# Performance work log

Measured on AMD Instinct MI355X. Metric: run time of the kernel, lower is better.

## Reference

```python
import jax, jax.numpy as jnp
import numpy as np

B, FIXED_LEN, N_FRAME, MID, P = 4096, 8192, 2112, 264, 88
UNROLLED_ITER = 5


def setup_inputs() -> dict:
    key = jax.random.key(0)
    ks = jax.random.split(key, 8)
    # Fourier weights scaled by 1/FIXED_LEN as in fourier_init
    W_cos = jax.random.normal(ks[0], (N_FRAME, FIXED_LEN), jnp.float32) / FIXED_LEN
    W_sin = jax.random.normal(ks[1], (N_FRAME, FIXED_LEN), jnp.float32) / FIXED_LEN
    # template is |cisoid_dict|^2 >= 0; small positive values keep the unrolled loop stable
    template = jax.random.uniform(ks[2], (N_FRAME, MID), jnp.float32) * 0.01
    return {
        "input_this": jax.random.normal(ks[3], (B, FIXED_LEN), jnp.float32),
        "input_prev": jax.random.normal(ks[4], (B, FIXED_LEN), jnp.float32),
        "W_cos": W_cos,
        "W_sin": W_sin,
        "template": template,
        "W1": jax.random.normal(ks[5], (MID, MID), jnp.float32) * 0.05 + jnp.eye(MID, dtype=jnp.float32),
        "b1": jnp.zeros((MID,), jnp.float32),
        "W2": jax.random.normal(ks[6], (P, MID), jnp.float32) * 0.1,
        "b2": jnp.zeros((P,), jnp.float32),
        "Wout": jax.random.normal(ks[7], (P, P), jnp.float32) * 0.1 + 4.0 * jnp.eye(P, dtype=jnp.float32),
        "bout": jnp.full((P,), -3.0, jnp.float32),
    }


def reference(input_this, input_prev, W_cos, W_sin, template, W1, b1, W2, b2, Wout, bout):
    fixed_len = jnp.asarray(input_this.shape[1], input_this.dtype)
    # get_feat: normalized power spectrum features
    n_valid = (jnp.count_nonzero(input_this, axis=1) + 1).astype(input_this.dtype)[:, None]
    scale = fixed_len / n_valid                      # [B, 1]
    x_cos = (input_this @ W_cos.T) * scale           # [B, N_FRAME]
    x_sin = (input_this @ W_sin.T) * scale
    feat = x_cos * x_cos + x_sin * x_sin             # [B, N_FRAME]

    # process_feat: unrolled LISTA-style iterations
    running = feat
    xi = -running
    m = jax.nn.relu(-10.0 * (xi @ template))         # [B, MID]
    for _ in range(UNROLLED_ITER - 1):
        xi = 1.6 * ((m @ template.T) - running) + 0.2 * xi
        m = jax.nn.relu(-8.0 * (xi @ template) + 0.2 * m)

    h = jax.nn.relu(jax.nn.relu(m @ W1.T + b1) @ W2.T + b2)  # [B, P]
    return jax.nn.sigmoid(h @ Wout.T + bout)         # velocity_estimate [B, P]
```

## Files before the change

kernel.cpp:

```cpp
#include <hip/hip_runtime.h>
#include <cstdint>
#include <cstddef>

#define B_SZ 4096
#define KLEN 8192
#define NF   2112
#define MID  264
#define PD   88

typedef _Float16 f16;
typedef _Float16 f16x4 __attribute__((ext_vector_type(4)));
typedef _Float16 f16x8 __attribute__((ext_vector_type(8)));
typedef float    f32x4 __attribute__((ext_vector_type(4)));

__device__ __forceinline__ void gl2lds16(const void* g, void* l) {
    __builtin_amdgcn_global_load_lds(
        (const __attribute__((address_space(1))) void*)g,
        (__attribute__((address_space(3))) void*)l, 16, 0, 0);
}

__global__ void k_row_prep(const float* __restrict__ x, f16* __restrict__ xh,
                           float* __restrict__ alpha) {
    const int row = blockIdx.x;
    const float* xr = x + (size_t)row * KLEN;
    f16* xhr = xh + (size_t)row * KLEN;
    int cnt = 0;
    for (int j = threadIdx.x * 4; j < KLEN; j += 256 * 4) {
        float4 v = *(const float4*)(xr + j);
        f16x4 h = { (f16)v.x, (f16)v.y, (f16)v.z, (f16)v.w };
        *(f16x4*)(xhr + j) = h;
        cnt += (v.x != 0.f) + (v.y != 0.f) + (v.z != 0.f) + (v.w != 0.f);
    }
    for (int off = 32; off > 0; off >>= 1) cnt += __shfl_down(cnt, off);
    __shared__ int lsum[4];
    if ((threadIdx.x & 63) == 0) lsum[threadIdx.x >> 6] = cnt;
    __syncthreads();
    if (threadIdx.x == 0)
        alpha[row] = 8.0f / (float)(lsum[0] + lsum[1] + lsum[2] + lsum[3] + 1);
}

__global__ void k_cvt_w2(const float* __restrict__ wc, const float* __restrict__ ws,
                         f16* __restrict__ whc, f16* __restrict__ whs, int n4) {
    const float* w = blockIdx.y ? ws : wc;
    f16* wh = blockIdx.y ? whs : whc;
    for (int i = blockIdx.x * blockDim.x + threadIdx.x; i < n4; i += gridDim.x * blockDim.x) {
        float4 v = ((const float4*)w)[i];
        f16x4 h = { (f16)(v.x * 8192.f), (f16)(v.y * 8192.f),
                    (f16)(v.z * 8192.f), (f16)(v.w * 8192.f) };
        ((f16x4*)wh)[i] = h;
    }
}

__global__ void k_prep_tt(const float* __restrict__ T, f16* __restrict__ tt) {
    __shared__ float tile[32][33];
    const int k0 = blockIdx.x * 32, n0 = blockIdx.y * 32;
    const int tx = threadIdx.x & 31, ty = threadIdx.x >> 5;
    for (int r = ty; r < 32; r += 8) {
        const int k = k0 + r, n = n0 + tx;
        tile[r][tx] = (n < MID) ? T[(size_t)k * MID + n] : 0.f;
    }
    __syncthreads();
    for (int r = ty; r < 32; r += 8) {
        const int n = n0 + r, k = k0 + tx;
        tt[(size_t)n * NF + k] = (f16)tile[tx][r];
    }
}

__global__ void k_gram(const float* __restrict__ T, float* __restrict__ G) {
    __shared__ float Pp[32][64];
    __shared__ float Qq[32][64];
    const int i0 = blockIdx.x * 64, j0 = blockIdx.y * 64;
    const int tx = threadIdx.x & 15, ty = threadIdx.x >> 4;
    float acc[4][4] = {};
    for (int kc = blockIdx.z * 11; kc < (int)blockIdx.z * 11 + 11; ++kc) {
        const int k0 = kc * 32;
        for (int l = threadIdx.x; l < 32 * 64; l += 256) {
            const int kk = l >> 6, cc = l & 63, kr = k0 + kk;
            Pp[kk][cc] = (i0 + cc < MID) ? T[(size_t)kr * MID + i0 + cc] : 0.f;
            Qq[kk][cc] = (j0 + cc < MID) ? T[(size_t)kr * MID + j0 + cc] : 0.f;
        }
        __syncthreads();
        for (int kk = 0; kk < 32; ++kk) {
            float a_[4], b_[4];
#pragma unroll
            for (int u = 0; u < 4; ++u) a_[u] = Pp[kk][tx * 4 + u];
#pragma unroll
            for (int w = 0; w < 4; ++w) b_[w] = Qq[kk][ty * 4 + w];
#pragma unroll
            for (int u = 0; u < 4; ++u)
#pragma unroll
                for (int w = 0; w < 4; ++w) acc[u][w] += a_[u] * b_[w];
        }
        __syncthreads();
    }
    for (int u = 0; u < 4; ++u) {
        const int gi = i0 + tx * 4 + u;
        if (gi >= MID) continue;
        for (int w = 0; w < 4; ++w) {
            const int gj = j0 + ty * 4 + w;
            if (gj < MID) atomicAdd(&G[(size_t)gi * MID + gj], acc[u][w]);
        }
    }
}

__global__ __launch_bounds__(256, 2) void k_fourier(
    const f16* __restrict__ A, const f16* __restrict__ Bc, const f16* __restrict__ Bs,
    const float* __restrict__ alpha, f16* __restrict__ feat) {
    __shared__ __align__(16) f16 As4[4][128 * 32];
    __shared__ __align__(16) f16 Bcs4[4][64 * 32];
    __shared__ __align__(16) f16 Bss4[4][64 * 32];
    const int tid = threadIdx.x, lane = tid & 63, wave = tid >> 6;
    const int wm = wave & 1, wn = wave >> 1;

    const int bid = blockIdx.y * 33 + blockIdx.x;
    const int swz = (bid & 7) * 132 + (bid >> 3);
    const int bx = swz % 33, by = swz / 33;
    const int m0 = by * 128, n0 = bx * 64;

    const int srow = tid >> 2;
    const int cswz = ((tid & 3) ^ ((tid >> 3) & 3)) << 3;
    const f16* pA  = A  + (size_t)(m0 + srow) * KLEN + cswz;
    const f16* pBc = Bc + (size_t)(n0 + srow) * KLEN + cswz;
    const f16* pBs = Bs + (size_t)(n0 + srow) * KLEN + cswz;

#define STAGE_F(h, b)                                                             \
    {                                                                             \
        gl2lds16(pA + (size_t)(h) * 32, (char*)&As4[b][0] + tid * 16);            \
        gl2lds16(pA + (size_t)64 * KLEN + (size_t)(h) * 32,                       \
                 (char*)&As4[b][0] + (tid + 256) * 16);                           \
        gl2lds16(pBc + (size_t)(h) * 32, (char*)&Bcs4[b][0] + tid * 16);          \
        gl2lds16(pBs + (size_t)(h) * 32, (char*)&Bss4[b][0] + tid * 16);          \
    }

    const int c0 = lane >> 4;
    int offA[4], offB[2];
#pragma unroll
    for (int mt = 0; mt < 4; ++mt) {
        const int r = wm * 64 + mt * 16 + (lane & 15);
        offA[mt] = r * 32 + ((c0 ^ ((r >> 1) & 3)) << 3);
    }
#pragma unroll
    for (int nt = 0; nt < 2; ++nt) {
        const int r = wn * 32 + nt * 16 + (lane & 15);
        offB[nt] = r * 32 + ((c0 ^ ((r >> 1) & 3)) << 3);
    }

    f32x4 accC[4][2], accS[4][2];
    const f32x4 z4 = {0.f, 0.f, 0.f, 0.f};
#pragma unroll
    for (int i = 0; i < 4; ++i)
#pragma unroll
        for (int j = 0; j < 2; ++j) { accC[i][j] = z4; accS[i][j] = z4; }

#define COMPUTE_F(b)                                                              \
    {                                                                             \
        f16x8 af[4], bcf[2], bsf[2];                                              \
        _Pragma("unroll")                                                         \
        for (int mt = 0; mt < 4; ++mt)                                            \
            af[mt] = *(const f16x8*)(&As4[b][offA[mt]]);                          \
        _Pragma("unroll")                                                         \
        for (int nt = 0; nt < 2; ++nt) {                                          \
            bcf[nt] = *(const f16x8*)(&Bcs4[b][offB[nt]]);                        \
            bsf[nt] = *(const f16x8*)(&Bss4[b][offB[nt]]);                        \
        }                                                                         \
        __builtin_amdgcn_s_setprio(1);                                            \
        _Pragma("unroll")                                                         \
        for (int mt = 0; mt < 4; ++mt)                                            \
            _Pragma("unroll")                                                     \
            for (int nt = 0; nt < 2; ++nt) {                                      \
                accC[mt][nt] = __builtin_amdgcn_mfma_f32_16x16x32_f16(            \
                    af[mt], bcf[nt], accC[mt][nt], 0, 0, 0);                      \
                accS[mt][nt] = __builtin_amdgcn_mfma_f32_16x16x32_f16(            \
                    af[mt], bsf[nt], accS[mt][nt], 0, 0, 0);                      \
            }                                                                     \
        __builtin_amdgcn_s_setprio(0);                                            \
    }

#define WAITB(n)                                                                  \
    asm volatile("s_waitcnt vmcnt(" #n ")" ::: "memory");                         \
    __builtin_amdgcn_s_barrier();

    STAGE_F(0, 0); STAGE_F(1, 1); STAGE_F(2, 2);
    WAITB(8);

#pragma unroll 1
    for (int h = 0; h < 252; h += 4) {
        STAGE_F(h + 3, 3); COMPUTE_F(0); WAITB(8);
        STAGE_F(h + 4, 0); COMPUTE_F(1); WAITB(8);
        STAGE_F(h + 5, 1); COMPUTE_F(2); WAITB(8);
        STAGE_F(h + 6, 2); COMPUTE_F(3); WAITB(8);
    }
    STAGE_F(255, 3); COMPUTE_F(0); WAITB(8);
    COMPUTE_F(1); WAITB(4);
    COMPUTE_F(2); WAITB(0);
    COMPUTE_F(3);
#undef STAGE_F
#undef COMPUTE_F
#undef WAITB

#pragma unroll
    for (int mt = 0; mt < 4; ++mt)
#pragma unroll
        for (int reg = 0; reg < 4; ++reg) {
            const int row = m0 + wm * 64 + mt * 16 + ((lane >> 4) << 2) + reg;
            const float al = alpha[row];
#pragma unroll
            for (int nt = 0; nt < 2; ++nt) {
                const int col = n0 + wn * 32 + nt * 16 + (lane & 15);
                const float xc = accC[mt][nt][reg] * al;
                const float xs = accS[mt][nt][reg] * al;
                feat[(size_t)row * NF + col] = (f16)(xc * xc + xs * xs);
            }
        }
}

__global__ __launch_bounds__(256, 2) void k_ggemm(
    const f16* __restrict__ A, const f16* __restrict__ Bt, float* __restrict__ g64) {
    __shared__ __align__(16) f16 As[2][128 * 64];
    __shared__ __align__(16) f16 Bs_[2][64 * 64];
    const int tid = threadIdx.x, lane = tid & 63, wave = tid >> 6;
    const int wm = wave & 1, wn = wave >> 1;
    const int m0 = blockIdx.y * 128, n0 = blockIdx.x * 64;
    const int srow = tid >> 3;
    const int scol = ((tid & 7) ^ (srow & 7)) << 3;
    const f16* gA = A + (size_t)(m0 + srow) * NF + scol;
    const f16* gB = Bt + (size_t)(n0 + srow) * NF + scol;

#define STAGE_G(buf, kq)                                                          \
    {                                                                             \
        _Pragma("unroll")                                                         \
        for (int i = 0; i < 4; ++i)                                               \
            gl2lds16(gA + (size_t)(32 * i) * NF + (kq),                           \
                     (char*)&As[buf][0] + (tid + 256 * i) * 16);                  \
        _Pragma("unroll")                                                         \
        for (int i = 0; i < 2; ++i)                                               \
            gl2lds16(gB + (size_t)(32 * i) * NF + (kq),                           \
                     (char*)&Bs_[buf][0] + (tid + 256 * i) * 16);                 \
    }

    f32x4 acc[4][2];
    const f32x4 z4 = {0.f, 0.f, 0.f, 0.f};
#pragma unroll
    for (int i = 0; i < 4; ++i)
#pragma unroll
        for (int j = 0; j < 2; ++j) acc[i][j] = z4;

    STAGE_G(0, 0);
    for (int k0 = 0; k0 < NF; k0 += 64) {
        const int cur = (k0 >> 6) & 1;
        __syncthreads();
        if (k0 + 64 < NF) STAGE_G(cur ^ 1, k0 + 64);
#pragma unroll
        for (int kk = 0; kk < 2; ++kk) {
            const int chunk0 = kk * 4 + (lane >> 4);
            f16x8 af[4], bf[2];
#pragma unroll
            for (int mt = 0; mt < 4; ++mt) {
                const int r = wm * 64 + mt * 16 + (lane & 15);
                af[mt] = *(const f16x8*)(&As[cur][0] + r * 64 + ((chunk0 ^ (r & 7)) << 3));
            }
#pragma unroll
            for (int nt = 0; nt < 2; ++nt) {
                const int r = wn * 32 + nt * 16 + (lane & 15);
                bf[nt] = *(const f16x8*)(&Bs_[cur][0] + r * 64 + ((chunk0 ^ (r & 7)) << 3));
            }
#pragma unroll
            for (int mt = 0; mt < 4; ++mt)
#pragma unroll
                for (int nt = 0; nt < 2; ++nt)
                    acc[mt][nt] = __builtin_amdgcn_mfma_f32_16x16x32_f16(af[mt], bf[nt], acc[mt][nt], 0, 0, 0);
        }
    }
#undef STAGE_G
#pragma unroll
    for (int mt = 0; mt < 4; ++mt)
#pragma unroll
        for (int reg = 0; reg < 4; ++reg) {
            const int row = m0 + wm * 64 + mt * 16 + ((lane >> 4) << 2) + reg;
#pragma unroll
            for (int nt = 0; nt < 2; ++nt) {
                const int col = n0 + wn * 32 + nt * 16 + (lane & 15);
                if (col < MID) g64[(size_t)row * MID + col] = acc[mt][nt][reg];
            }
        }
}

__global__ __launch_bounds__(320) void k_tail(
    const float* __restrict__ g64, const float* __restrict__ Gm,
    const float* __restrict__ W1, const float* __restrict__ b1,
    const float* __restrict__ W2, const float* __restrict__ b2,
    const float* __restrict__ Wout, const float* __restrict__ bout,
    float* __restrict__ out) {
    __shared__ __align__(16) float m_l[8 * 268];
    __shared__ __align__(16) float h2_l[8 * 92];
    const int t = threadIdx.x;
    const int r0 = blockIdx.x * 8;
    const bool act = (t < 264);
    const int rb = (t & 3) * 2;
    const int cb = (t >> 2) * 4;

    for (int idx = t; idx < 8 * MID; idx += 320) {
        const int r = idx / MID, c = idx - r * MID;
        const float gv = g64[(size_t)r0 * MID + idx] * 0.015625f;
        m_l[r * 268 + c] = fmaxf(10.f * gv, 0.f);
    }
    float gr[2][4], ur[2][4];
    if (act) {
#pragma unroll
        for (int u = 0; u < 2; ++u) {
            const float4 gq = *(const float4*)&g64[(size_t)(r0 + rb + u) * MID + cb];
            gr[u][0] = gq.x * 0.015625f; gr[u][1] = gq.y * 0.015625f;
            gr[u][2] = gq.z * 0.015625f; gr[u][3] = gq.w * 0.015625f;
#pragma unroll
            for (int j = 0; j < 4; ++j) ur[u][j] = -gr[u][j];
        }
    }
    __syncthreads();

    for (int it = 0; it < 4; ++it) {
        float v[2][4];
        if (act) {
#pragma unroll
            for (int u = 0; u < 2; ++u)
#pragma unroll
                for (int j = 0; j < 4; ++j) v[u][j] = 0.f;
            for (int k = 0; k < MID; k += 4) {
                float4 m4[2];
#pragma unroll
                for (int u = 0; u < 2; ++u) m4[u] = *(const float4*)&m_l[(rb + u) * 268 + k];
#pragma unroll
                for (int j = 0; j < 4; ++j) {
                    const float4 gv4 = *(const float4*)&Gm[(size_t)(cb + j) * MID + k];
#pragma unroll
                    for (int u = 0; u < 2; ++u)
                        v[u][j] += m4[u].x * gv4.x + m4[u].y * gv4.y + m4[u].z * gv4.z + m4[u].w * gv4.w;
                }
            }
        }
        __syncthreads();
        if (act) {
#pragma unroll
            for (int u = 0; u < 2; ++u)
#pragma unroll
                for (int j = 0; j < 4; ++j) {
                    const float un = 1.6f * (v[u][j] - gr[u][j]) + 0.2f * ur[u][j];
                    ur[u][j] = un;
                    float* mp = &m_l[(rb + u) * 268 + cb + j];
                    *mp = fmaxf(-8.f * un + 0.2f * (*mp), 0.f);
                }
        }
        __syncthreads();
    }

    {
        float v[2][4];
        if (act) {
#pragma unroll
            for (int u = 0; u < 2; ++u)
#pragma unroll
                for (int j = 0; j < 4; ++j) v[u][j] = 0.f;
            for (int k = 0; k < MID; k += 4) {
                float4 m4[2];
#pragma unroll
                for (int u = 0; u < 2; ++u) m4[u] = *(const float4*)&m_l[(rb + u) * 268 + k];
#pragma unroll
                for (int j = 0; j < 4; ++j) {
                    const float4 wv = *(const float4*)&W1[(size_t)(cb + j) * MID + k];
#pragma unroll
                    for (int u = 0; u < 2; ++u)
                        v[u][j] += m4[u].x * wv.x + m4[u].y * wv.y + m4[u].z * wv.z + m4[u].w * wv.w;
                }
            }
        }
        __syncthreads();
        if (act) {
#pragma unroll
            for (int u = 0; u < 2; ++u)
#pragma unroll
                for (int j = 0; j < 4; ++j)
                    m_l[(rb + u) * 268 + cb + j] = fmaxf(v[u][j] + b1[cb + j], 0.f);
        }
        __syncthreads();
    }

    const bool act2 = (t < 88);
    const int rb2 = (t & 3) * 2, cb2 = (t >> 2) * 4;
    if (act2) {
        float v[2][4];
#pragma unroll
        for (int u = 0; u < 2; ++u)
#pragma unroll
            for (int j = 0; j < 4; ++j) v[u][j] = 0.f;
        for (int k = 0; k < MID; k += 4) {
            float4 m4[2];
#pragma unroll
            for (int u = 0; u < 2; ++u) m4[u] = *(const float4*)&m_l[(rb2 + u) * 268 + k];
#pragma unroll
            for (int j = 0; j < 4; ++j) {
                const float4 wv = *(const float4*)&W2[(size_t)(cb2 + j) * MID + k];
#pragma unroll
                for (int u = 0; u < 2; ++u)
                    v[u][j] += m4[u].x * wv.x + m4[u].y * wv.y + m4[u].z * wv.z + m4[u].w * wv.w;
            }
        }
#pragma unroll
        for (int u = 0; u < 2; ++u)
#pragma unroll
            for (int j = 0; j < 4; ++j)
                h2_l[(rb2 + u) * 92 + cb2 + j] = fmaxf(v[u][j] + b2[cb2 + j], 0.f);
    }
    __syncthreads();
    if (act2) {
        float v[2][4];
#pragma unroll
        for (int u = 0; u < 2; ++u)
#pragma unroll
            for (int j = 0; j < 4; ++j) v[u][j] = 0.f;
        for (int q = 0; q < PD; q += 4) {
            float4 h4[2];
#pragma unroll
            for (int u = 0; u < 2; ++u) h4[u] = *(const float4*)&h2_l[(rb2 + u) * 92 + q];
#pragma unroll
            for (int j = 0; j < 4; ++j) {
                const float4 wv = *(const float4*)&Wout[(size_t)(cb2 + j) * PD + q];
#pragma unroll
                for (int u = 0; u < 2; ++u)
                    v[u][j] += h4[u].x * wv.x + h4[u].y * wv.y + h4[u].z * wv.z + h4[u].w * wv.w;
            }
        }
#pragma unroll
        for (int u = 0; u < 2; ++u) {
            float4 o;
            o.x = 1.f / (1.f + expf(-(v[u][0] + bout[cb2 + 0])));
            o.y = 1.f / (1.f + expf(-(v[u][1] + bout[cb2 + 1])));
            o.z = 1.f / (1.f + expf(-(v[u][2] + bout[cb2 + 2])));
            o.w = 1.f / (1.f + expf(-(v[u][3] + bout[cb2 + 3])));
            *(float4*)&out[(size_t)(r0 + rb2 + u) * PD + cb2] = o;
        }
    }
}

extern "C" void kernel_launch(void* const* d_in, const int* in_sizes, int n_in,
                              void* d_out, int out_size, void* d_ws, size_t ws_size,
                              hipStream_t stream) {
    (void)in_sizes; (void)n_in; (void)out_size; (void)ws_size;
    const float* inp  = (const float*)d_in[0];
    const float* wcos = (const float*)d_in[2];
    const float* wsin = (const float*)d_in[3];
    const float* tmpl = (const float*)d_in[4];
    const float* W1   = (const float*)d_in[5];
    const float* b1   = (const float*)d_in[6];
    const float* W2   = (const float*)d_in[7];
    const float* b2   = (const float*)d_in[8];
    const float* Wout = (const float*)d_in[9];
    const float* bout = (const float*)d_in[10];
    float* out = (float*)d_out;

    char* p = (char*)d_ws;
    f16* a_h    = (f16*)p;   p += (size_t)B_SZ * KLEN * 2;
    f16* wc_h   = (f16*)p;   p += (size_t)NF * KLEN * 2;
    f16* ws_h   = (f16*)p;   p += (size_t)NF * KLEN * 2;
    f16* feat_h = (f16*)p;   p += (size_t)B_SZ * NF * 2;
    f16* tt_h   = (f16*)p;   p += (size_t)320 * NF * 2;
    float* alpha= (float*)p; p += (size_t)B_SZ * 4;
    float* g64  = (float*)p; p += (size_t)B_SZ * MID * 4;
    float* Gm   = (float*)p; p += (size_t)MID * MID * 4;

    hipMemsetAsync(Gm, 0, (size_t)MID * MID * 4, stream);
    k_row_prep<<<B_SZ, 256, 0, stream>>>(inp, a_h, alpha);
    k_cvt_w2<<<dim3(2048, 2), 256, 0, stream>>>(wcos, wsin, wc_h, ws_h,
                                                (int)((size_t)NF * KLEN / 4));
    k_prep_tt<<<dim3(NF / 32, 10), 256, 0, stream>>>(tmpl, tt_h);
    k_gram<<<dim3(5, 5, 6), 256, 0, stream>>>(tmpl, Gm);
    k_fourier<<<dim3(NF / 64, B_SZ / 128), 256, 0, stream>>>(a_h, wc_h, ws_h, alpha, feat_h);
    k_ggemm<<<dim3(5, B_SZ / 128), 256, 0, stream>>>(feat_h, tt_h, g64);
    k_tail<<<B_SZ / 8, 320, 0, stream>>>(g64, Gm, W1, b1, W2, b2, Wout, bout, out);
}
```

Before: 1.098 ms.

## Switch Fourier GEMM to double-buffered LDS pipeline with higher occupancy

Cuts the Fourier GEMM's LDS staging from a 4-stage ring to 2 buffers, halving shared memory per block. Launch bounds go from 2 to 4 blocks per CU so more blocks can be resident. The loop is restructured into phases that prefetch the next tile, wait, barrier, compute and barrier again. More resident waves may hide memory latency better, but each block now has a shallower prefetch depth and an extra barrier per step, and the tighter register budget could cause spills.

```diff
diff --git a/kernel.cpp b/kernel.cpp
--- a/kernel.cpp
+++ b/kernel.cpp
@@ -103,12 +103,12 @@
     }
 }
 
-__global__ __launch_bounds__(256, 2) void k_fourier(
+__global__ __launch_bounds__(256, 4) void k_fourier(
     const f16* __restrict__ A, const f16* __restrict__ Bc, const f16* __restrict__ Bs,
     const float* __restrict__ alpha, f16* __restrict__ feat) {
-    __shared__ __align__(16) f16 As4[4][128 * 32];
-    __shared__ __align__(16) f16 Bcs4[4][64 * 32];
-    __shared__ __align__(16) f16 Bss4[4][64 * 32];
+    __shared__ __align__(16) f16 As2[2][128 * 32];
+    __shared__ __align__(16) f16 Bcs2[2][64 * 32];
+    __shared__ __align__(16) f16 Bss2[2][64 * 32];
     const int tid = threadIdx.x, lane = tid & 63, wave = tid >> 6;
     const int wm = wave & 1, wn = wave >> 1;
 
@@ -125,11 +125,11 @@
 
 #define STAGE_F(h, b)                                                             \
     {                                                                             \
-        gl2lds16(pA + (size_t)(h) * 32, (char*)&As4[b][0] + tid * 16);            \
+        gl2lds16(pA + (size_t)(h) * 32, (char*)&As2[b][0] + tid * 16);            \
         gl2lds16(pA + (size_t)64 * KLEN + (size_t)(h) * 32,                       \
-                 (char*)&As4[b][0] + (tid + 256) * 16);                           \
-        gl2lds16(pBc + (size_t)(h) * 32, (char*)&Bcs4[b][0] + tid * 16);          \
-        gl2lds16(pBs + (size_t)(h) * 32, (char*)&Bss4[b][0] + tid * 16);          \
+                 (char*)&As2[b][0] + (tid + 256) * 16);                           \
+        gl2lds16(pBc + (size_t)(h) * 32, (char*)&Bcs2[b][0] + tid * 16);          \
+        gl2lds16(pBs + (size_t)(h) * 32, (char*)&Bss2[b][0] + tid * 16);          \
     }
 
     const int c0 = lane >> 4;
@@ -157,11 +157,11 @@
         f16x8 af[4], bcf[2], bsf[2];                                              \
         _Pragma("unroll")                                                         \
         for (int mt = 0; mt < 4; ++mt)                                            \
-            af[mt] = *(const f16x8*)(&As4[b][offA[mt]]);                          \
+            af[mt] = *(const f16x8*)(&As2[b][offA[mt]]);                          \
         _Pragma("unroll")                                                         \
         for (int nt = 0; nt < 2; ++nt) {                                          \
-            bcf[nt] = *(const f16x8*)(&Bcs4[b][offB[nt]]);                        \
-            bsf[nt] = *(const f16x8*)(&Bss4[b][offB[nt]]);                        \
+            bcf[nt] = *(const f16x8*)(&Bcs2[b][offB[nt]]);                        \
+            bsf[nt] = *(const f16x8*)(&Bss2[b][offB[nt]]);                        \
         }                                                                         \
         __builtin_amdgcn_s_setprio(1);                                            \
         _Pragma("unroll")                                                         \
@@ -176,27 +176,26 @@
         __builtin_amdgcn_s_setprio(0);                                            \
     }
 
-#define WAITB(n)                                                                  \
-    asm volatile("s_waitcnt vmcnt(" #n ")" ::: "memory");                         \
+#define PHASE_F(h, bc, bn)                                                        \
+    STAGE_F((h) + 1, bn);                                                         \
+    asm volatile("s_waitcnt vmcnt(4)" ::: "memory");                              \
+    __builtin_amdgcn_s_barrier();                                                 \
+    COMPUTE_F(bc);                                                                \
     __builtin_amdgcn_s_barrier();
 
-    STAGE_F(0, 0); STAGE_F(1, 1); STAGE_F(2, 2);
-    WAITB(8);
-
+    STAGE_F(0, 0);
 #pragma unroll 1
-    for (int h = 0; h < 252; h += 4) {
-        STAGE_F(h + 3, 3); COMPUTE_F(0); WAITB(8);
-        STAGE_F(h + 4, 0); COMPUTE_F(1); WAITB(8);
-        STAGE_F(h + 5, 1); COMPUTE_F(2); WAITB(8);
-        STAGE_F(h + 6, 2); COMPUTE_F(3); WAITB(8);
-    }
-    STAGE_F(255, 3); COMPUTE_F(0); WAITB(8);
-    COMPUTE_F(1); WAITB(4);
-    COMPUTE_F(2); WAITB(0);
-    COMPUTE_F(3);
+    for (int h = 0; h < 254; h += 2) {
+        PHASE_F(h, 0, 1)
+        PHASE_F(h + 1, 1, 0)
+    }
+    PHASE_F(254, 0, 1)
+    asm volatile("s_waitcnt vmcnt(0)" ::: "memory");
+    __builtin_amdgcn_s_barrier();
+    COMPUTE_F(1);
 #undef STAGE_F
 #undef COMPUTE_F
-#undef WAITB
+#undef PHASE_F
 
 #pragma unroll
     for (int mt = 0; mt < 4; ++mt)
```

After: 1.032 ms. 6.0% less time.
